# Kernel optimization log

Hardware: AMD Instinct MI355X
Metric: run time of the kernel (lower is better)

## Reference

```python
import jax, jax.numpy as jnp
import numpy as np

HEADS = 8
EPS = 1e-5
PW1 = (512, 8, 14, 14)   # (C, T, H, W), C = headsize1 * heads
PW2 = (512, 32, 7, 7)


def _ln(x, g, b):
    m = jnp.mean(x, axis=-1, keepdims=True)
    v = jnp.var(x, axis=-1, keepdims=True)
    return (x - m) * jax.lax.rsqrt(v + EPS) * g + b


def _mha(q, k, v):
    b, nq, c = q.shape
    nk = k.shape[1]
    hd = c // HEADS
    qh = q.reshape(b, nq, HEADS, hd).transpose(0, 2, 1, 3)  # [b,h,nq,hd]
    kh = k.reshape(b, nk, HEADS, hd).transpose(0, 2, 1, 3)
    vh = v.reshape(b, nk, HEADS, hd).transpose(0, 2, 1, 3)
    s = jnp.einsum('bhqd,bhkd->bhqk', qh, kh) * (hd ** -0.5)
    a = jax.nn.softmax(s, axis=-1)
    o = jnp.einsum('bhqk,bhkd->bhqd', a, vh)
    return o.transpose(0, 2, 1, 3).reshape(b, nq, c)


def _tok(x):
    b, c, t, h, w = x.shape
    return x.transpose(0, 2, 3, 4, 1).reshape(b, t * h * w, c)


def _detok(t, c, T, H, W):
    b = t.shape[0]
    return t.reshape(b, T, H, W, c).transpose(0, 4, 1, 2, 3)


def _out_head(y, w, bias, bn_g, bn_b):
    # 1x1x1 Conv3d + ReLU + BatchNorm3d (eval, running mean 0 / var 1)
    z = jnp.einsum('bcthw,oc->bothw', y, w) + bias[None, :, None, None, None]
    z = jax.nn.relu(z)
    z = z * jax.lax.rsqrt(jnp.float32(1.0 + EPS))
    return z * bn_g[None, :, None, None, None] + bn_b[None, :, None, None, None]


def reference(x1, x2, Wq1, bq1, Wk1, bk1, Wv1, bv1, ln1_g, ln1_b,
              Wq2, bq2, Wk2, bk2, Wv2, bv2, ln2_g, ln2_b,
              out1_w, out1_b, bn1_g, bn1_b, out2_w, out2_b, bn2_g, bn2_b):
    t1 = _tok(x1)  # [B, 1568, 512]
    t2 = _tok(x2)  # [B, 1568, 512]
    for i in range(3):  # three chained norm + cross-attn stages
        q1 = _ln(t1, ln1_g[i], ln1_b[i]) @ Wq1[i].T + bq1[i]
        k1 = t2 @ Wk1[i].T + bk1[i]
        v1 = t2 @ Wv1[i].T + bv1[i]
        q2 = _ln(t2, ln2_g[i], ln2_b[i]) @ Wq2[i].T + bq2[i]
        k2 = t1 @ Wk2[i].T + bk2[i]
        v2 = t1 @ Wv2[i].T + bv2[i]
        t1 = t1 + _mha(q1, k1, v1)
        t2 = t2 + _mha(q2, k2, v2)
    y1 = _detok(t1, *PW1)
    y2 = _detok(t2, *PW2)
    z1 = _out_head(y1, out1_w, out1_b, bn1_g, bn1_b)
    z2 = _out_head(y2, out2_w, out2_b, bn2_g, bn2_b)
    return (z1, z2)


def setup_inputs() -> dict:
    key = jax.random.key(0)
    ks = jax.random.split(key, 12)
    C = 512
    w = lambda k, shp: jax.random.normal(k, shp, jnp.float32) * 0.02
    return {
        'x1': jax.random.normal(ks[0], (4, C, 8, 14, 14), jnp.float32),
        'x2': jax.random.normal(ks[1], (4, C, 32, 7, 7), jnp.float32),
        'Wq1': w(ks[2], (3, C, C)), 'bq1': jnp.zeros((3, C), jnp.float32),
        'Wk1': w(ks[3], (3, C, C)), 'bk1': jnp.zeros((3, C), jnp.float32),
        'Wv1': w(ks[4], (3, C, C)), 'bv1': jnp.zeros((3, C), jnp.float32),
        'ln1_g': jnp.ones((3, C), jnp.float32), 'ln1_b': jnp.zeros((3, C), jnp.float32),
        'Wq2': w(ks[5], (3, C, C)), 'bq2': jnp.zeros((3, C), jnp.float32),
        'Wk2': w(ks[6], (3, C, C)), 'bk2': jnp.zeros((3, C), jnp.float32),
        'Wv2': w(ks[7], (3, C, C)), 'bv2': jnp.zeros((3, C), jnp.float32),
        'ln2_g': jnp.ones((3, C), jnp.float32), 'ln2_b': jnp.zeros((3, C), jnp.float32),
        'out1_w': w(ks[8], (C, C)), 'out1_b': jnp.zeros((C,), jnp.float32),
        'bn1_g': jnp.ones((C,), jnp.float32), 'bn1_b': jnp.zeros((C,), jnp.float32),
        'out2_w': w(ks[9], (C, C)), 'out2_b': jnp.zeros((C,), jnp.float32),
        'bn2_g': jnp.ones((C,), jnp.float32), 'bn2_b': jnp.zeros((C,), jnp.float32),
    }
```

## Files before the change

kernel.cpp:

```cpp
#include <hip/hip_runtime.h>

typedef __bf16 bf16_t;
typedef __bf16 bf16x8 __attribute__((ext_vector_type(8)));
typedef __bf16 bf16x4 __attribute__((ext_vector_type(4)));
typedef float f32x4 __attribute__((ext_vector_type(4)));
typedef float f32x16 __attribute__((ext_vector_type(16)));
typedef unsigned u32x4 __attribute__((ext_vector_type(4)));

#define NTOK 1568
#define CDIM 512
#define BATCH 4
#define MROWS (BATCH*NTOK)
#define RSQ1PEPS 0.9999950000374997f
#define CEXP 0.1803368801111204f

__device__ __forceinline__ float fexp2(float x) {
  float r;
  asm("v_exp_f32 %0, %1" : "=v"(r) : "v"(x));
  return r;
}

__device__ __forceinline__ void glds16(const bf16_t* src, bf16_t* dst) {
  __builtin_amdgcn_global_load_lds(
      (const __attribute__((address_space(1))) unsigned*)src,
      (__attribute__((address_space(3))) unsigned*)dst, 16, 0, 0);
}

struct CastArgs { const float* s[20]; };
__global__ __launch_bounds__(256) void cast_kernel(CastArgs ca, bf16_t* __restrict__ out) {
  int idx = blockIdx.x * 256 + threadIdx.x;
  int m = idx >> 16;
  const float4* sp = (const float4*)ca.s[m];
  float4 v = sp[idx & 65535];
  bf16x4 o;
  o[0] = (bf16_t)v.x; o[1] = (bf16_t)v.y; o[2] = (bf16_t)v.z; o[3] = (bf16_t)v.w;
  *(bf16x4*)(out + (size_t)idx * 4) = o;
}

struct TokArgs { const float* x[2]; float* tf[2]; bf16_t* tb[2]; };
__global__ __launch_bounds__(256) void tok_kernel(TokArgs ta) {
  __shared__ float tile[32][33];
  int z = blockIdx.z, sel = z >> 2, b = z & 3;
  int c0 = blockIdx.y * 32, s0 = blockIdx.x * 32;
  int tx = threadIdx.x, ty = threadIdx.y;
  const float* xp = ta.x[sel] + (size_t)b * CDIM * NTOK;
  for (int r = 0; r < 32; r += 8)
    tile[ty + r][tx] = xp[(size_t)(c0 + ty + r) * NTOK + s0 + tx];
  __syncthreads();
  float* tfp = ta.tf[sel] + (size_t)b * NTOK * CDIM;
  bf16_t* tbp = ta.tb[sel] + (size_t)b * NTOK * CDIM;
  for (int r = 0; r < 32; r += 8) {
    float v = tile[tx][ty + r];
    size_t idx = (size_t)(s0 + ty + r) * CDIM + c0 + tx;
    tfp[idx] = v;
    tbp[idx] = (bf16_t)v;
  }
}

__global__ __launch_bounds__(64) void ln_kernel(
    const float* __restrict__ t1, const float* __restrict__ t2,
    const float* __restrict__ g1, const float* __restrict__ b1,
    const float* __restrict__ g2, const float* __restrict__ b2,
    bf16_t* __restrict__ o1, bf16_t* __restrict__ o2) {
  int row = blockIdx.x;
  const float* t; const float* g; const float* bt; bf16_t* out;
  if (row < MROWS) { t = t1; g = g1; bt = b1; out = o1; }
  else { row -= MROWS; t = t2; g = g2; bt = b2; out = o2; }
  int l = threadIdx.x;
  const float* x = t + (size_t)row * CDIM;
  float4 v0 = ((const float4*)x)[l];
  float4 v1 = ((const float4*)x)[l + 64];
  float s = v0.x + v0.y + v0.z + v0.w + v1.x + v1.y + v1.z + v1.w;
  float sq = v0.x*v0.x + v0.y*v0.y + v0.z*v0.z + v0.w*v0.w
           + v1.x*v1.x + v1.y*v1.y + v1.z*v1.z + v1.w*v1.w;
  for (int m = 1; m < 64; m <<= 1) { s += __shfl_xor(s, m); sq += __shfl_xor(sq, m); }
  float mean = s * (1.f / 512.f);
  float var = sq * (1.f / 512.f) - mean * mean;
  float rs = rsqrtf(var + 1e-5f);
  float4 g0 = ((const float4*)g)[l], g1v = ((const float4*)g)[l + 64];
  float4 b0 = ((const float4*)bt)[l], b1v = ((const float4*)bt)[l + 64];
  bf16x4 o0, o1v;
  o0[0] = (bf16_t)((v0.x - mean) * rs * g0.x + b0.x);
  o0[1] = (bf16_t)((v0.y - mean) * rs * g0.y + b0.y);
  o0[2] = (bf16_t)((v0.z - mean) * rs * g0.z + b0.z);
  o0[3] = (bf16_t)((v0.w - mean) * rs * g0.w + b0.w);
  o1v[0] = (bf16_t)((v1.x - mean) * rs * g1v.x + b1v.x);
  o1v[1] = (bf16_t)((v1.y - mean) * rs * g1v.y + b1v.y);
  o1v[2] = (bf16_t)((v1.z - mean) * rs * g1v.z + b1v.z);
  o1v[3] = (bf16_t)((v1.w - mean) * rs * g1v.w + b1v.w);
  *(bf16x4*)(out + (size_t)row * CDIM + l * 4) = o0;
  *(bf16x4*)(out + (size_t)row * CDIM + 256 + l * 4) = o1v;
}

template<int MODE>
__device__ __forceinline__ void gemm_core(
    bf16_t (* __restrict__ As)[40], bf16_t (* __restrict__ Bs)[40],
    const bf16_t* __restrict__ A, const bf16_t* __restrict__ Bp,
    const float* __restrict__ bias, const float* __restrict__ bng,
    const float* __restrict__ bnb, bf16_t* __restrict__ outb,
    float* __restrict__ outf, int m0, int n0, int Nvalid, float scl) {
  int tid = threadIdx.x;
  int w = tid >> 6, l = tid & 63, lr = l & 15, kg = l >> 4;
  int wm = (w >> 1) * 64, wn = (w & 1) * 64;
  f32x4 acc[4][4];
  for (int i = 0; i < 4; i++)
    for (int j = 0; j < 4; j++)
      acc[i][j] = f32x4{0.f, 0.f, 0.f, 0.f};
  int srow = tid >> 1;
  int soff = (tid & 1) * 16;
  int brow = n0 + srow;
  if (MODE != 0 && brow >= Nvalid) brow = Nvalid - 1;
  const bf16_t* aq = A + (size_t)(m0 + srow) * CDIM + soff;
  const bf16_t* bq = Bp + (size_t)brow * CDIM + soff;
  for (int kk = 0; kk < 16; kk++) {
    __syncthreads();
    bf16x8 a0 = *(const bf16x8*)(aq);
    bf16x8 a1 = *(const bf16x8*)(aq + 8);
    bf16x8 b0 = *(const bf16x8*)(bq);
    bf16x8 b1 = *(const bf16x8*)(bq + 8);
    aq += 32; bq += 32;
    *(bf16x8*)&As[srow][soff] = a0;
    *(bf16x8*)&As[srow][soff + 8] = a1;
    *(bf16x8*)&Bs[srow][soff] = b0;
    *(bf16x8*)&Bs[srow][soff + 8] = b1;
    __syncthreads();
    bf16x8 af[4], bfr[4];
    for (int i = 0; i < 4; i++) af[i] = *(const bf16x8*)&As[wm + i * 16 + lr][kg * 8];
    for (int j = 0; j < 4; j++) bfr[j] = *(const bf16x8*)&Bs[wn + j * 16 + lr][kg * 8];
    for (int i = 0; i < 4; i++)
      for (int j = 0; j < 4; j++)
        acc[i][j] = __builtin_amdgcn_mfma_f32_16x16x32_bf16(af[i], bfr[j], acc[i][j], 0, 0, 0);
  }
  for (int i = 0; i < 4; i++)
    for (int j = 0; j < 4; j++) {
      int rbase = m0 + wm + i * 16 + kg * 4;
      int col = n0 + wn + j * 16 + lr;
      for (int r = 0; r < 4; r++) {
        int row = rbase + r;
        float v = acc[i][j][r];
        if (MODE == 0) {
          v = (v + bias[col]) * scl;
          outb[(size_t)row * CDIM + col] = (bf16_t)v;
        } else if (MODE == 1) {
          v += bias[row];
          v = v > 0.f ? v : 0.f;
          v *= RSQ1PEPS;
          v = v * bng[row] + bnb[row];
          if (col < Nvalid) outf[(size_t)row * NTOK + col] = v;
        } else {
          v += bias[row];
          if (col < Nvalid) outb[(size_t)row * NTOK + col] = (bf16_t)v;
        }
      }
    }
}

struct ProjArgs {
  const bf16_t* A0[4]; const bf16_t* W0[4]; const float* b0[4]; bf16_t* o0[4];
  float scl0[4];
  const bf16_t* W2[2]; const bf16_t* B2[2]; const float* b2[2]; bf16_t* o2[2];
};
__global__ __launch_bounds__(256) void proj_kernel(ProjArgs p) {
  __shared__ bf16_t As[128][40];
  __shared__ bf16_t Bs[128][40];
  int id = blockIdx.x;
  if (id < 784) {
    int set = id / 196, rem = id % 196;
    int n0 = (rem & 3) * 128, m0 = (rem >> 2) * 128;
    gemm_core<0>(As, Bs, p.A0[set], p.W0[set], p.b0[set], nullptr, nullptr,
                 p.o0[set], nullptr, m0, n0, 512, p.scl0[set]);
  } else {
    int j = id - 784;
    int unit = j / 52;
    int which = unit >> 2, bat = unit & 3;
    int rem = j % 52;
    int n0 = (rem % 13) * 128, m0 = (rem / 13) * 128;
    gemm_core<2>(As, Bs, p.W2[which], p.B2[which] + (size_t)bat * NTOK * CDIM,
                 p.b2[which], nullptr, nullptr,
                 p.o2[which] + (size_t)bat * CDIM * NTOK, nullptr, m0, n0, NTOK, 1.f);
  }
}

__global__ __launch_bounds__(256) void head_kernel(
    const bf16_t* __restrict__ W1, const bf16_t* __restrict__ W2,
    const bf16_t* __restrict__ t1b, const bf16_t* __restrict__ t2b,
    const float* __restrict__ b1, const float* __restrict__ b2,
    const float* __restrict__ bng1, const float* __restrict__ bnb1,
    const float* __restrict__ bng2, const float* __restrict__ bnb2,
    float* __restrict__ out) {
  __shared__ bf16_t As[128][40];
  __shared__ bf16_t Bs[128][40];
  int z = blockIdx.z;
  int which = z >> 2, bat = z & 3;
  const bf16_t* A = which ? W2 : W1;
  const bf16_t* Bp = (which ? t2b : t1b) + (size_t)bat * NTOK * CDIM;
  const float* bias = which ? b2 : b1;
  const float* bng = which ? bng2 : bng1;
  const float* bnb = which ? bnb2 : bnb1;
  float* outf = out + (size_t)which * BATCH * CDIM * NTOK + (size_t)bat * CDIM * NTOK;
  int m0 = blockIdx.y * 128, n0 = blockIdx.x * 128;
  gemm_core<1>(As, Bs, A, Bp, bias, bng, bnb, nullptr, outf, m0, n0, NTOK, 1.f);
}

__device__ __forceinline__ void build_frags(const float* p, bf16x8& Fa, bf16x8& Fb) {
  unsigned pk[8];
#pragma unroll
  for (int g = 0; g < 8; g++) {
    union { bf16_t hh[2]; unsigned u; } cv;
    cv.hh[0] = (bf16_t)p[2 * g];
    cv.hh[1] = (bf16_t)p[2 * g + 1];
    pk[g] = cv.u;
  }
  asm volatile("v_permlane32_swap_b32 %0, %1" : "+v"(pk[0]), "+v"(pk[2]));
  asm volatile("v_permlane32_swap_b32 %0, %1" : "+v"(pk[1]), "+v"(pk[3]));
  asm volatile("v_permlane32_swap_b32 %0, %1" : "+v"(pk[4]), "+v"(pk[6]));
  asm volatile("v_permlane32_swap_b32 %0, %1" : "+v"(pk[5]), "+v"(pk[7]));
  union { u32x4 u; bf16x8 bv; } A, B;
  A.u[0] = pk[0]; A.u[1] = pk[1]; A.u[2] = pk[2]; A.u[3] = pk[3];
  B.u[0] = pk[4]; B.u[1] = pk[5]; B.u[2] = pk[6]; B.u[3] = pk[7];
  Fa = A.bv; Fb = B.bv;
}

struct AttnArgs {
  const bf16_t* q[2]; const bf16_t* k[2]; const bf16_t* v[2];
  float* tf[2]; bf16_t* tb[2];
};

#define STAGE(TN, SL)                                                         \
  {                                                                           \
    int tnS_ = (TN); if (tnS_ > 48) tnS_ = 48;                                \
    glds16(kgl + (size_t)tnS_ * (32 * CDIM), &Ks[SL][wq8][0]);                \
    glds16(vgl + tnS_ * 32, &Vs[SL][wq16][0]);                                \
  }

#define QK(SL, SA)                                                            \
  {                                                                           \
    const bf16_t* kr_ = &Ks[SL][lo][0];                                       \
    __builtin_amdgcn_s_setprio(1);                                            \
    SA = __builtin_amdgcn_mfma_f32_32x32x16_bf16(                             \
        *(const bf16x8*)(kr_ + ((hi * 8) ^ sw3)), qf[0], z, 0, 0, 0);         \
    SA = __builtin_amdgcn_mfma_f32_32x32x16_bf16(                             \
        *(const bf16x8*)(kr_ + ((16 + hi * 8) ^ sw3)), qf[1], SA, 0, 0, 0);   \
    SA = __builtin_amdgcn_mfma_f32_32x32x16_bf16(                             \
        *(const bf16x8*)(kr_ + ((32 + hi * 8) ^ sw3)), qf[2], SA, 0, 0, 0);   \
    SA = __builtin_amdgcn_mfma_f32_32x32x16_bf16(                             \
        *(const bf16x8*)(kr_ + ((48 + hi * 8) ^ sw3)), qf[3], SA, 0, 0, 0);   \
    __builtin_amdgcn_s_setprio(0);                                            \
  }

#define FIN(SA, SL)                                                           \
  {                                                                           \
    float pa_[16];                                                            \
    _Pragma("unroll")                                                         \
    for (int r_ = 0; r_ < 16; r_++) pa_[r_] = fexp2(SA[r_]);                  \
    bf16x8 F0_, F1_;                                                          \
    build_frags(pa_, F0_, F1_);                                               \
    __builtin_amdgcn_s_setprio(1);                                            \
    ls = __builtin_amdgcn_mfma_f32_32x32x16_bf16(kone, F0_, ls, 0, 0, 0);     \
    ls = __builtin_amdgcn_mfma_f32_32x32x16_bf16(kone, F1_, ls, 0, 0, 0);     \
    ot0 = __builtin_amdgcn_mfma_f32_32x32x16_bf16(                            \
        *(const bf16x8*)(&Vs[SL][lo][(hi * 8) ^ sw2]), F0_, ot0, 0, 0, 0);    \
    ot0 = __builtin_amdgcn_mfma_f32_32x32x16_bf16(                            \
        *(const bf16x8*)(&Vs[SL][lo][(16 + hi * 8) ^ sw2]), F1_, ot0, 0, 0, 0);\
    ot1 = __builtin_amdgcn_mfma_f32_32x32x16_bf16(                            \
        *(const bf16x8*)(&Vs[SL][32 + lo][(hi * 8) ^ sw2]), F0_, ot1, 0, 0, 0);\
    ot1 = __builtin_amdgcn_mfma_f32_32x32x16_bf16(                            \
        *(const bf16x8*)(&Vs[SL][32 + lo][(16 + hi * 8) ^ sw2]), F1_, ot1, 0, 0, 0);\
    __builtin_amdgcn_s_setprio(0);                                            \
  }

#define STEP(T, SACUR, SAPRV, QSL, FSL, SSL)                                  \
  {                                                                           \
    STAGE((T) + 2, SSL);                                                      \
    QK(QSL, SACUR);                                                           \
    FIN(SAPRV, FSL);                                                          \
    asm volatile("s_waitcnt vmcnt(3)" ::: "memory");                          \
    __builtin_amdgcn_s_barrier();                                             \
  }

__global__ __launch_bounds__(256) void attn_kernel(AttnArgs aa) {
  __shared__ alignas(16) bf16_t Ks[4][32][64];
  __shared__ alignas(16) bf16_t Vs[4][64][32];
  int id = blockIdx.x;
  int xcd = id & 7, sl = id >> 3;
  int g = xcd + ((sl / 13) << 3);
  int qt = sl % 13;
  int ss = g >> 5, b = (g >> 3) & 3, h = g & 7;
  const bf16_t* qg = aa.q[ss];
  const bf16_t* kgp = aa.k[ss];
  const bf16_t* vtg = aa.v[ss];
  float* tf = aa.tf[ss];
  bf16_t* tb = aa.tb[ss];
  int tid = threadIdx.x, w = tid >> 6, l = tid & 63;
  int lo = l & 31, hi = l >> 5;
  int wq8 = w * 8, wq16 = w * 16;
  int sw3 = (lo & 7) << 3;
  int sw2 = ((lo >> 1) & 3) << 3;
  const size_t kbase = ((size_t)b * NTOK) * CDIM + h * 64;
  const size_t vbase = ((size_t)b * CDIM + h * 64) * NTOK;

  int q0 = qt * 128 + w * 32;
  int qrow = q0 + lo;
  int qr = qrow < NTOK ? qrow : NTOK - 1;
  const bf16_t* qp = qg + kbase + (size_t)qr * CDIM + hi * 8;
  bf16x8 qf[4];
  qf[0] = *(const bf16x8*)(qp);
  qf[1] = *(const bf16x8*)(qp + 16);
  qf[2] = *(const bf16x8*)(qp + 32);
  qf[3] = *(const bf16x8*)(qp + 48);
  asm volatile("" : "+v"(qf[0]), "+v"(qf[1]), "+v"(qf[2]), "+v"(qf[3]));
  asm volatile("s_waitcnt vmcnt(0)" ::: "memory");

  const bf16_t* kgl = kgp + kbase + (size_t)(wq8 + (l >> 3)) * CDIM
                      + (((l & 7) ^ ((l >> 3) & 7)) << 3);
  const bf16_t* vgl = vtg + vbase + (size_t)(wq16 + (l >> 2)) * NTOK
                      + (((l & 3) ^ ((l >> 3) & 3)) << 3);

  bf16x8 kone;
#pragma unroll
  for (int j = 0; j < 8; j++) kone[j] = (bf16_t)1.0f;

  f32x16 ot0, ot1, ls, z, saA, saB;
#pragma unroll
  for (int r = 0; r < 16; r++) { ot0[r] = 0.f; ot1[r] = 0.f; ls[r] = 0.f; z[r] = 0.f; }

  STAGE(0, 0);
  STAGE(1, 1);
  STAGE(2, 2);
  asm volatile("s_waitcnt vmcnt(2)" ::: "memory");
  __builtin_amdgcn_s_barrier();
  QK(0, saA);

  for (int t = 1; t <= 45; t += 4) {
    STEP(t + 0, saB, saA, 1, 0, 3);
    STEP(t + 1, saA, saB, 2, 1, 0);
    STEP(t + 2, saB, saA, 3, 2, 1);
    STEP(t + 3, saA, saB, 0, 3, 2);
  }
  FIN(saA, 0);

  if (qrow < NTOK) {
    float inv = 1.f / ls[0];
    float* tfp = tf + ((size_t)b * NTOK + qrow) * CDIM + h * 64 + hi * 4;
    bf16_t* tbp = tb + ((size_t)b * NTOK + qrow) * CDIM + h * 64 + hi * 4;
#pragma unroll
    for (int db = 0; db < 2; db++) {
#pragma unroll
      for (int gq = 0; gq < 4; gq++) {
        int doff = db * 32 + gq * 8;
        float4 old = *(float4*)(tfp + doff);
        float4 nv;
        float a0 = (db ? ot1[gq * 4 + 0] : ot0[gq * 4 + 0]) * inv;
        float a1 = (db ? ot1[gq * 4 + 1] : ot0[gq * 4 + 1]) * inv;
        float a2 = (db ? ot1[gq * 4 + 2] : ot0[gq * 4 + 2]) * inv;
        float a3 = (db ? ot1[gq * 4 + 3] : ot0[gq * 4 + 3]) * inv;
        nv.x = old.x + a0; nv.y = old.y + a1; nv.z = old.z + a2; nv.w = old.w + a3;
        *(float4*)(tfp + doff) = nv;
        bf16x4 ob;
        ob[0] = (bf16_t)nv.x; ob[1] = (bf16_t)nv.y;
        ob[2] = (bf16_t)nv.z; ob[3] = (bf16_t)nv.w;
        *(bf16x4*)(tbp + doff) = ob;
      }
    }
  }
}

extern "C" void kernel_launch(void* const* d_in, const int* in_sizes, int n_in,
                              void* d_out, int out_size, void* d_ws, size_t ws_size,
                              hipStream_t stream) {
  (void)in_sizes; (void)n_in; (void)out_size; (void)ws_size;
  const float* x1 = (const float*)d_in[0];
  const float* x2 = (const float*)d_in[1];
  const float* Wq1 = (const float*)d_in[2];
  const float* bq1 = (const float*)d_in[3];
  const float* Wk1 = (const float*)d_in[4];
  const float* bk1 = (const float*)d_in[5];
  const float* Wv1 = (const float*)d_in[6];
  const float* bv1 = (const float*)d_in[7];
  const float* ln1_g = (const float*)d_in[8];
  const float* ln1_b = (const float*)d_in[9];
  const float* Wq2 = (const float*)d_in[10];
  const float* bq2 = (const float*)d_in[11];
  const float* Wk2 = (const float*)d_in[12];
  const float* bk2 = (const float*)d_in[13];
  const float* Wv2 = (const float*)d_in[14];
  const float* bv2 = (const float*)d_in[15];
  const float* ln2_g = (const float*)d_in[16];
  const float* ln2_b = (const float*)d_in[17];
  const float* out1_w = (const float*)d_in[18];
  const float* out1_b = (const float*)d_in[19];
  const float* bn1_g = (const float*)d_in[20];
  const float* bn1_b = (const float*)d_in[21];
  const float* out2_w = (const float*)d_in[22];
  const float* out2_b = (const float*)d_in[23];
  const float* bn2_g = (const float*)d_in[24];
  const float* bn2_b = (const float*)d_in[25];

  const size_t WMAT = 512 * 512;
  char* ws = (char*)d_ws;
  bf16_t* wb = (bf16_t*)ws;
  size_t off = 20 * WMAT * sizeof(bf16_t);
  float* t1f = (float*)(ws + off); off += (size_t)MROWS * CDIM * 4;
  float* t2f = (float*)(ws + off); off += (size_t)MROWS * CDIM * 4;
  bf16_t* t1b = (bf16_t*)(ws + off); off += (size_t)MROWS * CDIM * 2;
  bf16_t* t2b = (bf16_t*)(ws + off); off += (size_t)MROWS * CDIM * 2;
  bf16_t* l1b = (bf16_t*)(ws + off); off += (size_t)MROWS * CDIM * 2;
  bf16_t* l2b = (bf16_t*)(ws + off); off += (size_t)MROWS * CDIM * 2;
  bf16_t* q1b = (bf16_t*)(ws + off); off += (size_t)MROWS * CDIM * 2;
  bf16_t* k1b = (bf16_t*)(ws + off); off += (size_t)MROWS * CDIM * 2;
  bf16_t* v1b = (bf16_t*)(ws + off); off += (size_t)MROWS * CDIM * 2;
  bf16_t* q2b = (bf16_t*)(ws + off); off += (size_t)MROWS * CDIM * 2;
  bf16_t* k2b = (bf16_t*)(ws + off); off += (size_t)MROWS * CDIM * 2;
  bf16_t* v2b = (bf16_t*)(ws + off); off += (size_t)MROWS * CDIM * 2;

  CastArgs ca;
  for (int i = 0; i < 3; i++) {
    ca.s[0 + i] = Wq1 + (size_t)i * WMAT;
    ca.s[3 + i] = Wk1 + (size_t)i * WMAT;
    ca.s[6 + i] = Wv1 + (size_t)i * WMAT;
    ca.s[9 + i] = Wq2 + (size_t)i * WMAT;
    ca.s[12 + i] = Wk2 + (size_t)i * WMAT;
    ca.s[15 + i] = Wv2 + (size_t)i * WMAT;
  }
  ca.s[18] = out1_w;
  ca.s[19] = out2_w;
  cast_kernel<<<5120, 256, 0, stream>>>(ca, wb);

  TokArgs ta;
  ta.x[0] = x1; ta.x[1] = x2;
  ta.tf[0] = t1f; ta.tf[1] = t2f;
  ta.tb[0] = t1b; ta.tb[1] = t2b;
  tok_kernel<<<dim3(49, 16, 8), dim3(32, 8), 0, stream>>>(ta);

  AttnArgs aa;
  aa.q[0] = q1b; aa.q[1] = q2b;
  aa.k[0] = k1b; aa.k[1] = k2b;
  aa.v[0] = v1b; aa.v[1] = v2b;
  aa.tf[0] = t1f; aa.tf[1] = t2f;
  aa.tb[0] = t1b; aa.tb[1] = t2b;

  for (int i = 0; i < 3; i++) {
    ln_kernel<<<2 * MROWS, 64, 0, stream>>>(t1f, t2f,
        ln1_g + i * 512, ln1_b + i * 512, ln2_g + i * 512, ln2_b + i * 512,
        l1b, l2b);
    ProjArgs pa;
    pa.A0[0] = l1b; pa.W0[0] = wb + (0 + i) * WMAT; pa.b0[0] = bq1 + i * 512; pa.o0[0] = q1b;
    pa.A0[1] = t2b; pa.W0[1] = wb + (3 + i) * WMAT; pa.b0[1] = bk1 + i * 512; pa.o0[1] = k1b;
    pa.A0[2] = l2b; pa.W0[2] = wb + (9 + i) * WMAT; pa.b0[2] = bq2 + i * 512; pa.o0[2] = q2b;
    pa.A0[3] = t1b; pa.W0[3] = wb + (12 + i) * WMAT; pa.b0[3] = bk2 + i * 512; pa.o0[3] = k2b;
    pa.scl0[0] = CEXP; pa.scl0[1] = 1.f; pa.scl0[2] = CEXP; pa.scl0[3] = 1.f;
    pa.W2[0] = wb + (6 + i) * WMAT; pa.B2[0] = t2b; pa.b2[0] = bv1 + i * 512; pa.o2[0] = v1b;
    pa.W2[1] = wb + (15 + i) * WMAT; pa.B2[1] = t1b; pa.b2[1] = bv2 + i * 512; pa.o2[1] = v2b;
    proj_kernel<<<1200, 256, 0, stream>>>(pa);
    attn_kernel<<<832, 256, 0, stream>>>(aa);
  }

  float* out = (float*)d_out;
  head_kernel<<<dim3(13, 4, 8), 256, 0, stream>>>(
      wb + 18 * WMAT, wb + 19 * WMAT, t1b, t2b,
      out1_b, out2_b, bn1_g, bn1_b, bn2_g, bn2_b, out);
}
```

Measured before the change: 398.0 us.

## Process two query tiles per attention block to reuse staged K/V tiles

```diff
diff --git a/kernel.cpp b/kernel.cpp
--- a/kernel.cpp
+++ b/kernel.cpp
@@ -233,48 +233,61 @@
     glds16(vgl + tnS_ * 32, &Vs[SL][wq16][0]);                                \
   }
 
-#define QK(SL, SA)                                                            \
+#define QK2(SL)                                                               \
   {                                                                           \
     const bf16_t* kr_ = &Ks[SL][lo][0];                                       \
+    bf16x8 k0_ = *(const bf16x8*)(kr_ + ((hi * 8) ^ sw3));                    \
+    bf16x8 k1_ = *(const bf16x8*)(kr_ + ((16 + hi * 8) ^ sw3));               \
+    bf16x8 k2_ = *(const bf16x8*)(kr_ + ((32 + hi * 8) ^ sw3));               \
+    bf16x8 k3_ = *(const bf16x8*)(kr_ + ((48 + hi * 8) ^ sw3));               \
     __builtin_amdgcn_s_setprio(1);                                            \
-    SA = __builtin_amdgcn_mfma_f32_32x32x16_bf16(                             \
-        *(const bf16x8*)(kr_ + ((hi * 8) ^ sw3)), qf[0], z, 0, 0, 0);         \
-    SA = __builtin_amdgcn_mfma_f32_32x32x16_bf16(                             \
-        *(const bf16x8*)(kr_ + ((16 + hi * 8) ^ sw3)), qf[1], SA, 0, 0, 0);   \
-    SA = __builtin_amdgcn_mfma_f32_32x32x16_bf16(                             \
-        *(const bf16x8*)(kr_ + ((32 + hi * 8) ^ sw3)), qf[2], SA, 0, 0, 0);   \
-    SA = __builtin_amdgcn_mfma_f32_32x32x16_bf16(                             \
-        *(const bf16x8*)(kr_ + ((48 + hi * 8) ^ sw3)), qf[3], SA, 0, 0, 0);   \
+    saA = __builtin_amdgcn_mfma_f32_32x32x16_bf16(k0_, qfA[0], z, 0, 0, 0);   \
+    saB = __builtin_amdgcn_mfma_f32_32x32x16_bf16(k0_, qfB[0], z, 0, 0, 0);   \
+    saA = __builtin_amdgcn_mfma_f32_32x32x16_bf16(k1_, qfA[1], saA, 0, 0, 0); \
+    saB = __builtin_amdgcn_mfma_f32_32x32x16_bf16(k1_, qfB[1], saB, 0, 0, 0); \
+    saA = __builtin_amdgcn_mfma_f32_32x32x16_bf16(k2_, qfA[2], saA, 0, 0, 0); \
+    saB = __builtin_amdgcn_mfma_f32_32x32x16_bf16(k2_, qfB[2], saB, 0, 0, 0); \
+    saA = __builtin_amdgcn_mfma_f32_32x32x16_bf16(k3_, qfA[3], saA, 0, 0, 0); \
+    saB = __builtin_amdgcn_mfma_f32_32x32x16_bf16(k3_, qfB[3], saB, 0, 0, 0); \
     __builtin_amdgcn_s_setprio(0);                                            \
   }
 
-#define FIN(SA, SL)                                                           \
+#define FIN2(SL)                                                              \
   {                                                                           \
-    float pa_[16];                                                            \
+    float pa_[16], pb_[16];                                                   \
     _Pragma("unroll")                                                         \
-    for (int r_ = 0; r_ < 16; r_++) pa_[r_] = fexp2(SA[r_]);                  \
-    bf16x8 F0_, F1_;                                                          \
-    build_frags(pa_, F0_, F1_);                                               \
+    for (int r_ = 0; r_ < 16; r_++) pa_[r_] = fexp2(saA[r_]);                 \
+    _Pragma("unroll")                                                         \
+    for (int r_ = 0; r_ < 16; r_++) pb_[r_] = fexp2(saB[r_]);                 \
+    bf16x8 FA0_, FA1_, FB0_, FB1_;                                            \
+    build_frags(pa_, FA0_, FA1_);                                             \
+    build_frags(pb_, FB0_, FB1_);                                             \
+    bf16x8 v0_ = *(const bf16x8*)(&Vs[SL][lo][(hi * 8) ^ sw2]);               \
+    bf16x8 v1_ = *(const bf16x8*)(&Vs[SL][lo][(16 + hi * 8) ^ sw2]);          \
+    bf16x8 v2_ = *(const bf16x8*)(&Vs[SL][32 + lo][(hi * 8) ^ sw2]);          \
+    bf16x8 v3_ = *(const bf16x8*)(&Vs[SL][32 + lo][(16 + hi * 8) ^ sw2]);     \
     __builtin_amdgcn_s_setprio(1);                                            \
-    ls = __builtin_amdgcn_mfma_f32_32x32x16_bf16(kone, F0_, ls, 0, 0, 0);     \
-    ls = __builtin_amdgcn_mfma_f32_32x32x16_bf16(kone, F1_, ls, 0, 0, 0);     \
-    ot0 = __builtin_amdgcn_mfma_f32_32x32x16_bf16(                            \
-        *(const bf16x8*)(&Vs[SL][lo][(hi * 8) ^ sw2]), F0_, ot0, 0, 0, 0);    \
-    ot0 = __builtin_amdgcn_mfma_f32_32x32x16_bf16(                            \
-        *(const bf16x8*)(&Vs[SL][lo][(16 + hi * 8) ^ sw2]), F1_, ot0, 0, 0, 0);\
-    ot1 = __builtin_amdgcn_mfma_f32_32x32x16_bf16(                            \
-        *(const bf16x8*)(&Vs[SL][32 + lo][(hi * 8) ^ sw2]), F0_, ot1, 0, 0, 0);\
-    ot1 = __builtin_amdgcn_mfma_f32_32x32x16_bf16(                            \
-        *(const bf16x8*)(&Vs[SL][32 + lo][(16 + hi * 8) ^ sw2]), F1_, ot1, 0, 0, 0);\
+    lsA = __builtin_amdgcn_mfma_f32_32x32x16_bf16(kone, FA0_, lsA, 0, 0, 0);  \
+    lsB = __builtin_amdgcn_mfma_f32_32x32x16_bf16(kone, FB0_, lsB, 0, 0, 0);  \
+    lsA = __builtin_amdgcn_mfma_f32_32x32x16_bf16(kone, FA1_, lsA, 0, 0, 0);  \
+    lsB = __builtin_amdgcn_mfma_f32_32x32x16_bf16(kone, FB1_, lsB, 0, 0, 0);  \
+    otA0 = __builtin_amdgcn_mfma_f32_32x32x16_bf16(v0_, FA0_, otA0, 0, 0, 0); \
+    otB0 = __builtin_amdgcn_mfma_f32_32x32x16_bf16(v0_, FB0_, otB0, 0, 0, 0); \
+    otA0 = __builtin_amdgcn_mfma_f32_32x32x16_bf16(v1_, FA1_, otA0, 0, 0, 0); \
+    otB0 = __builtin_amdgcn_mfma_f32_32x32x16_bf16(v1_, FB1_, otB0, 0, 0, 0); \
+    otA1 = __builtin_amdgcn_mfma_f32_32x32x16_bf16(v2_, FA0_, otA1, 0, 0, 0); \
+    otB1 = __builtin_amdgcn_mfma_f32_32x32x16_bf16(v2_, FB0_, otB1, 0, 0, 0); \
+    otA1 = __builtin_amdgcn_mfma_f32_32x32x16_bf16(v3_, FA1_, otA1, 0, 0, 0); \
+    otB1 = __builtin_amdgcn_mfma_f32_32x32x16_bf16(v3_, FB1_, otB1, 0, 0, 0); \
     __builtin_amdgcn_s_setprio(0);                                            \
   }
 
-#define STEP(T, SACUR, SAPRV, QSL, FSL, SSL)                                  \
+#define STEPX(T, CUR, SSL)                                                    \
   {                                                                           \
     STAGE((T) + 2, SSL);                                                      \
-    QK(QSL, SACUR);                                                           \
-    FIN(SAPRV, FSL);                                                          \
-    asm volatile("s_waitcnt vmcnt(3)" ::: "memory");                          \
+    QK2(CUR);                                                                 \
+    FIN2(CUR);                                                                \
+    asm volatile("s_waitcnt vmcnt(2)" ::: "memory");                          \
     __builtin_amdgcn_s_barrier();                                             \
   }
 
@@ -283,8 +296,8 @@
   __shared__ alignas(16) bf16_t Vs[4][64][32];
   int id = blockIdx.x;
   int xcd = id & 7, sl = id >> 3;
-  int g = xcd + ((sl / 13) << 3);
-  int qt = sl % 13;
+  int g = xcd + ((sl / 7) << 3);
+  int blk = sl % 7;
   int ss = g >> 5, b = (g >> 3) & 3, h = g & 7;
   const bf16_t* qg = aa.q[ss];
   const bf16_t* kgp = aa.k[ss];
@@ -299,16 +312,24 @@
   const size_t kbase = ((size_t)b * NTOK) * CDIM + h * 64;
   const size_t vbase = ((size_t)b * CDIM + h * 64) * NTOK;
 
-  int q0 = qt * 128 + w * 32;
-  int qrow = q0 + lo;
-  int qr = qrow < NTOK ? qrow : NTOK - 1;
-  const bf16_t* qp = qg + kbase + (size_t)qr * CDIM + hi * 8;
-  bf16x8 qf[4];
-  qf[0] = *(const bf16x8*)(qp);
-  qf[1] = *(const bf16x8*)(qp + 16);
-  qf[2] = *(const bf16x8*)(qp + 32);
-  qf[3] = *(const bf16x8*)(qp + 48);
-  asm volatile("" : "+v"(qf[0]), "+v"(qf[1]), "+v"(qf[2]), "+v"(qf[3]));
+  int q0a = blk * 256 + w * 32;
+  int q0b = q0a + 128;
+  int qrowA = q0a + lo, qrowB = q0b + lo;
+  int qrA = qrowA < NTOK ? qrowA : NTOK - 1;
+  int qrB = qrowB < NTOK ? qrowB : NTOK - 1;
+  const bf16_t* qpA = qg + kbase + (size_t)qrA * CDIM + hi * 8;
+  const bf16_t* qpB = qg + kbase + (size_t)qrB * CDIM + hi * 8;
+  bf16x8 qfA[4], qfB[4];
+  qfA[0] = *(const bf16x8*)(qpA);
+  qfA[1] = *(const bf16x8*)(qpA + 16);
+  qfA[2] = *(const bf16x8*)(qpA + 32);
+  qfA[3] = *(const bf16x8*)(qpA + 48);
+  qfB[0] = *(const bf16x8*)(qpB);
+  qfB[1] = *(const bf16x8*)(qpB + 16);
+  qfB[2] = *(const bf16x8*)(qpB + 32);
+  qfB[3] = *(const bf16x8*)(qpB + 48);
+  asm volatile("" : "+v"(qfA[0]), "+v"(qfA[1]), "+v"(qfA[2]), "+v"(qfA[3]));
+  asm volatile("" : "+v"(qfB[0]), "+v"(qfB[1]), "+v"(qfB[2]), "+v"(qfB[3]));
   asm volatile("s_waitcnt vmcnt(0)" ::: "memory");
 
   const bf16_t* kgl = kgp + kbase + (size_t)(wq8 + (l >> 3)) * CDIM
@@ -320,29 +341,34 @@
 #pragma unroll
   for (int j = 0; j < 8; j++) kone[j] = (bf16_t)1.0f;
 
-  f32x16 ot0, ot1, ls, z, saA, saB;
-#pragma unroll
-  for (int r = 0; r < 16; r++) { ot0[r] = 0.f; ot1[r] = 0.f; ls[r] = 0.f; z[r] = 0.f; }
+  f32x16 otA0, otA1, otB0, otB1, lsA, lsB, z, saA, saB;
+#pragma unroll
+  for (int r = 0; r < 16; r++) {
+    otA0[r] = 0.f; otA1[r] = 0.f; otB0[r] = 0.f; otB1[r] = 0.f;
+    lsA[r] = 0.f; lsB[r] = 0.f; z[r] = 0.f;
+  }
 
   STAGE(0, 0);
   STAGE(1, 1);
-  STAGE(2, 2);
   asm volatile("s_waitcnt vmcnt(2)" ::: "memory");
   __builtin_amdgcn_s_barrier();
-  QK(0, saA);
-
-  for (int t = 1; t <= 45; t += 4) {
-    STEP(t + 0, saB, saA, 1, 0, 3);
-    STEP(t + 1, saA, saB, 2, 1, 0);
-    STEP(t + 2, saB, saA, 3, 2, 1);
-    STEP(t + 3, saA, saB, 0, 3, 2);
-  }
-  FIN(saA, 0);
-
-  if (qrow < NTOK) {
-    float inv = 1.f / ls[0];
-    float* tfp = tf + ((size_t)b * NTOK + qrow) * CDIM + h * 64 + hi * 4;
-    bf16_t* tbp = tb + ((size_t)b * NTOK + qrow) * CDIM + h * 64 + hi * 4;
+
+  for (int t = 0; t < 48; t += 4) {
+    STEPX(t + 0, 0, 2);
+    STEPX(t + 1, 1, 3);
+    STEPX(t + 2, 2, 0);
+    STEPX(t + 3, 3, 1);
+  }
+  QK2(0);
+  FIN2(0);
+  asm volatile("s_waitcnt vmcnt(0)" ::: "memory");
+
+  float* tfb = tf + (size_t)b * NTOK * CDIM + h * 64 + hi * 4;
+  bf16_t* tbb = tb + (size_t)b * NTOK * CDIM + h * 64 + hi * 4;
+  if (qrowA < NTOK) {
+    float inv = 1.f / lsA[0];
+    float* tfp = tfb + (size_t)qrowA * CDIM;
+    bf16_t* tbp = tbb + (size_t)qrowA * CDIM;
 #pragma unroll
     for (int db = 0; db < 2; db++) {
 #pragma unroll
@@ -350,10 +376,34 @@
         int doff = db * 32 + gq * 8;
         float4 old = *(float4*)(tfp + doff);
         float4 nv;
-        float a0 = (db ? ot1[gq * 4 + 0] : ot0[gq * 4 + 0]) * inv;
-        float a1 = (db ? ot1[gq * 4 + 1] : ot0[gq * 4 + 1]) * inv;
-        float a2 = (db ? ot1[gq * 4 + 2] : ot0[gq * 4 + 2]) * inv;
-        float a3 = (db ? ot1[gq * 4 + 3] : ot0[gq * 4 + 3]) * inv;
+        float a0 = (db ? otA1[gq * 4 + 0] : otA0[gq * 4 + 0]) * inv;
+        float a1 = (db ? otA1[gq * 4 + 1] : otA0[gq * 4 + 1]) * inv;
+        float a2 = (db ? otA1[gq * 4 + 2] : otA0[gq * 4 + 2]) * inv;
+        float a3 = (db ? otA1[gq * 4 + 3] : otA0[gq * 4 + 3]) * inv;
+        nv.x = old.x + a0; nv.y = old.y + a1; nv.z = old.z + a2; nv.w = old.w + a3;
+        *(float4*)(tfp + doff) = nv;
+        bf16x4 ob;
+        ob[0] = (bf16_t)nv.x; ob[1] = (bf16_t)nv.y;
+        ob[2] = (bf16_t)nv.z; ob[3] = (bf16_t)nv.w;
+        *(bf16x4*)(tbp + doff) = ob;
+      }
+    }
+  }
+  if (qrowB < NTOK) {
+    float inv = 1.f / lsB[0];
+    float* tfp = tfb + (size_t)qrowB * CDIM;
+    bf16_t* tbp = tbb + (size_t)qrowB * CDIM;
+#pragma unroll
+    for (int db = 0; db < 2; db++) {
+#pragma unroll
+      for (int gq = 0; gq < 4; gq++) {
+        int doff = db * 32 + gq * 8;
+        float4 old = *(float4*)(tfp + doff);
+        float4 nv;
+        float a0 = (db ? otB1[gq * 4 + 0] : otB0[gq * 4 + 0]) * inv;
+        float a1 = (db ? otB1[gq * 4 + 1] : otB0[gq * 4 + 1]) * inv;
+        float a2 = (db ? otB1[gq * 4 + 2] : otB0[gq * 4 + 2]) * inv;
+        float a3 = (db ? otB1[gq * 4 + 3] : otB0[gq * 4 + 3]) * inv;
         nv.x = old.x + a0; nv.y = old.y + a1; nv.z = old.z + a2; nv.w = old.w + a3;
         *(float4*)(tfp + doff) = nv;
         bf16x4 ob;
@@ -452,7 +502,7 @@
     pa.W2[0] = wb + (6 + i) * WMAT; pa.B2[0] = t2b; pa.b2[0] = bv1 + i * 512; pa.o2[0] = v1b;
     pa.W2[1] = wb + (15 + i) * WMAT; pa.B2[1] = t1b; pa.b2[1] = bv2 + i * 512; pa.o2[1] = v2b;
     proj_kernel<<<1200, 256, 0, stream>>>(pa);
-    attn_kernel<<<832, 256, 0, stream>>>(aa);
+    attn_kernel<<<448, 256, 0, stream>>>(aa);
   }
 
   float* out = (float*)d_out;
```

Result: slower. 530.6 us (+33.3%).
